# Optimization experiments

Measured on AMD Instinct MI355X. Metric: run time of the kernel, lower is better.

Reference implementation:

```python
import jax, jax.numpy as jnp
import numpy as np

B, LQ, LK = 64, 128, 1024
E, H = 768, 6
HD = E // H            # 128
D2 = HD // 2           # 64
LNUM = 2
QD, KD = 768, 768
EPS = 1e-5


def _gn(x, g, b):
    # torch.nn.GroupNorm(H, E) on 2D input [N, E]: normalize per group of HD channels
    N = x.shape[0]
    xg = x.reshape(N, H, HD)
    m = xg.mean(-1, keepdims=True)
    v = xg.var(-1, keepdims=True)
    xn = ((xg - m) / jnp.sqrt(v + EPS)).reshape(N, E)
    return xn * g + b


def _ln(x, g, b):
    m = x.mean(-1, keepdims=True)
    v = x.var(-1, keepdims=True)
    return (x - m) / jnp.sqrt(v + EPS) * g + b


def setup_inputs() -> dict:
    key = jax.random.key(0)
    ks = iter(jax.random.split(key, 64))
    def rn(shape, s=0.02):
        return jax.random.normal(next(ks), shape, dtype=jnp.float32) * s
    L = LNUM
    inp = {}
    inp['q_feat'] = jax.random.normal(next(ks), (B, LQ, QD), dtype=jnp.float32)
    inp['k_feats'] = jax.random.normal(next(ks), (B, LK, KD), dtype=jnp.float32)
    inp['q_mask'] = jnp.ones((B, LQ), jnp.float32)
    inp['k_mask'] = jnp.ones((B, LK), jnp.float32)
    # per-layer projections (stacked along layer axis)
    inp['Wq'] = rn((L, QD, E)); inp['bq'] = jnp.zeros((L, E)); inp['gq_g'] = jnp.ones((L, E)); inp['gq_b'] = jnp.zeros((L, E))
    inp['Wk'] = rn((L, KD, E)); inp['bk'] = jnp.zeros((L, E)); inp['gk_g'] = jnp.ones((L, E)); inp['gk_b'] = jnp.zeros((L, E))
    inp['Wv1'] = rn((L, QD, E)); inp['bv1'] = jnp.zeros((L, E)); inp['g1_g'] = jnp.ones((L, E)); inp['g1_b'] = jnp.zeros((L, E))
    inp['Wv2'] = rn((L, KD, E)); inp['bv2'] = jnp.zeros((L, E)); inp['g2_g'] = jnp.ones((L, E)); inp['g2_b'] = jnp.zeros((L, E))
    # inner Attention net (per layer)
    inp['Wab'] = rn((L, HD, D2)); inp['bab'] = jnp.zeros((L, D2))
    inp['Wal'] = rn((L, D2, 1)); inp['bal'] = jnp.zeros((L, 1))
    inp['Wac'] = rn((L, D2, HD)); inp['bac'] = jnp.zeros((L, HD))
    # bifeat_emb + layer norms (layer_num-1 of them)
    inp['Wbi'] = rn((L - 1, 2 * E, E)); inp['bbi'] = jnp.zeros((L - 1, E))
    inp['lnb_g'] = jnp.ones((L - 1, E)); inp['lnb_b'] = jnp.zeros((L - 1, E))
    # final proj + layernorm
    inp['Wp'] = rn((E * L + QD, E)); inp['bp'] = jnp.zeros((E,))
    inp['ln_g'] = jnp.ones((E,)); inp['ln_b'] = jnp.zeros((E,))
    return inp


def _bilinear_attention(q, k, kmask, p):
    (Wq, bq, gqg, gqb, Wk, bk, gkg, gkb, Wv1, bv1, g1g, g1b,
     Wv2, bv2, g2g, g2b, Wab, bab, Wal, bal, Wac, bac) = p
    Bb = q.shape[0]
    Lk = k.shape[1]
    qp = _gn(jnp.tanh(q @ Wq + bq), gqg, gqb).reshape(Bb, H, HD)      # [B,H,HD]
    v1 = _gn(jnp.tanh(q @ Wv1 + bv1), g1g, g1b).reshape(Bb, H, HD)
    kf = k.reshape(-1, k.shape[-1])
    kp = _gn(jnp.tanh(kf @ Wk + bk), gkg, gkb).reshape(Bb, Lk, H, HD).transpose(0, 2, 1, 3)   # [B,H,Lk,HD]
    v2 = _gn(jnp.tanh(kf @ Wv2 + bv2), g2g, g2b).reshape(Bb, Lk, H, HD).transpose(0, 2, 1, 3)
    att_map = qp[:, :, None, :] * kp                                  # [B,H,Lk,HD] bilinear map
    basic = jax.nn.relu(att_map @ Wab + bab)                          # [B,H,Lk,D2]
    mext = kmask[:, None, :, None]                                    # [B,1,Lk,1]
    pool = (basic * mext).sum(2) / mext.sum(2)                        # masked mean -> [B,H,D2]
    a_s = (basic @ Wal + bal)[..., 0]                                 # [B,H,Lk]
    a_s = jnp.where(kmask[:, None, :] == 0, -1e9, a_s)
    a_s = jax.nn.softmax(a_s, axis=-1)
    a_c = jax.nn.sigmoid(pool @ Wac + bac)                            # [B,H,HD] channel gate
    v2a = jnp.einsum('bhl,bhld->bhd', a_s, v2)
    return (v1 * v2a * a_c).reshape(Bb, E)


def reference(q_feat, k_feats, q_mask, k_mask,
              Wq, bq, gq_g, gq_b, Wk, bk, gk_g, gk_b,
              Wv1, bv1, g1_g, g1_b, Wv2, bv2, g2_g, g2_b,
              Wab, bab, Wal, bal, Wac, bac,
              Wbi, bbi, lnb_g, lnb_b, Wp, bp, ln_g, ln_b):
    qm = q_mask[..., None]
    q = (q_feat * qm).sum(1) / qm.sum(1)                              # masked mean pool -> [B,QD]
    feats = [q]
    k = k_feats
    for i in range(LNUM):
        p = (Wq[i], bq[i], gq_g[i], gq_b[i], Wk[i], bk[i], gk_g[i], gk_b[i],
             Wv1[i], bv1[i], g1_g[i], g1_b[i], Wv2[i], bv2[i], g2_g[i], g2_b[i],
             Wab[i], bab[i], Wal[i], bal[i], Wac[i], bac[i])
        q = _bilinear_attention(q, k, k_mask, p)                      # dropout = identity (eval)
        feats.append(q)
        if i < LNUM - 1:
            cat = jnp.concatenate([jnp.broadcast_to(q[:, None, :], k.shape), k], axis=-1)
            k = _ln(jax.nn.relu(cat @ Wbi[i] + bbi[i]) + k, lnb_g[i], lnb_b[i])
    out = _ln(jnp.concatenate(feats, axis=-1) @ Wp + bp, ln_g, ln_b)
    return out
```

## Files before the change

kernel.cpp:

```cpp
#include <hip/hip_runtime.h>
#include <math.h>

#define DEVI static __device__ __forceinline__

typedef unsigned short u16;
typedef __attribute__((ext_vector_type(8))) short short8;
typedef __attribute__((ext_vector_type(4))) float f32x4;

DEVI float bf2f(u16 u) { union { float f; unsigned int i; } c; c.i = ((unsigned int)u) << 16; return c.f; }
DEVI u16 f2bf(float f) {
  union { float f; unsigned int i; } c; c.f = f;
  unsigned int r = c.i + 0x7FFFu + ((c.i >> 16) & 1u);
  return (u16)(r >> 16);
}

DEVI float ftanh(float x) {
  float e = __expf(2.f * x);
  return 1.f - 2.f * __builtin_amdgcn_rcpf(e + 1.f);
}

DEVI void gld16(const u16* g, u16* l) {
  __builtin_amdgcn_global_load_lds((const __attribute__((address_space(1))) unsigned int*)g,
                                   (__attribute__((address_space(3))) unsigned int*)l, 16, 0, 0);
}

#define BB 64
#define LQN 128
#define LKN 1024
#define EN 768
#define HN 6
#define HDN 128
#define D2N 64
#define EPSV 1e-5f

#define NB_CONV 3072
#define NB_TW5 2880
#define NB_WAB 16
#define NB_UV 96
#define NB_PQ 64
#define NB_MS 64
#define NB_PREP (NB_CONV + NB_TW5 + NB_WAB + NB_UV + NB_PQ + NB_MS)

__global__ __launch_bounds__(256) void prep_kernel(
    const float* __restrict__ k_feats, u16* __restrict__ kf,
    const float* __restrict__ Wk, const float* __restrict__ Wv2,
    const float* __restrict__ Wbi, const float* __restrict__ lnb_g,
    u16* __restrict__ WkvT, u16* __restrict__ WbiT,
    const float* __restrict__ Wab, u16* __restrict__ WabT,
    const float* __restrict__ lnb_b, const float* __restrict__ bkL1,
    const float* __restrict__ bv2L1, float* __restrict__ uvec,
    float* __restrict__ vbvec,
    const float* __restrict__ qf, const float* __restrict__ qm,
    float* __restrict__ q_cur, float* __restrict__ feats,
    const float* __restrict__ km, float* __restrict__ msum) {
  __shared__ float ls[1056];
  int b = blockIdx.x, t = threadIdx.x;

  if (b < NB_CONV) {
    size_t n8 = (size_t)BB * LKN * EN / 8;
    for (size_t i = (size_t)b * 256 + t; i < n8; i += (size_t)NB_CONV * 256) {
      float4 a = ((const float4*)k_feats)[2 * i];
      float4 c = ((const float4*)k_feats)[2 * i + 1];
      short8 o;
      o[0] = (short)f2bf(a.x); o[1] = (short)f2bf(a.y); o[2] = (short)f2bf(a.z); o[3] = (short)f2bf(a.w);
      o[4] = (short)f2bf(c.x); o[5] = (short)f2bf(c.y); o[6] = (short)f2bf(c.z); o[7] = (short)f2bf(c.w);
      *(short8*)&kf[i * 8] = o;
    }
    return;
  }
  b -= NB_CONV;
  if (b < NB_TW5) {
    int z = b / 576, rem = b % 576;
    int kb = (rem / 24) * 32, nb = (rem % 24) * 32;
    const float* src;
    u16* dst;
    bool fold = (z == 1) || (z == 3);
    if (z < 2) { src = Wk + (size_t)z * EN * EN; dst = WkvT + (size_t)z * 1536 * EN; }
    else if (z < 4) { src = Wv2 + (size_t)(z - 2) * EN * EN; dst = WkvT + (size_t)(z - 2) * 1536 * EN + (size_t)EN * EN; }
    else { src = Wbi + (size_t)EN * EN; dst = WbiT; }
    int tx = t & 31, ty = t >> 5;
    for (int j = 0; j < 32; j += 8) {
      float v = src[(size_t)(kb + ty + j) * EN + nb + tx];
      if (fold) v *= lnb_g[kb + ty + j];
      ls[(ty + j) * 33 + tx] = v;
    }
    __syncthreads();
    for (int j = 0; j < 32; j += 8)
      dst[(size_t)(nb + ty + j) * EN + kb + tx] = f2bf(ls[tx * 33 + ty + j]);
    return;
  }
  b -= NB_TW5;
  if (b < NB_WAB) {
    int z = b / 8, rem = b % 8;
    int kb = (rem / 2) * 32, nb = (rem % 2) * 32;
    const float* src = Wab + (size_t)z * HDN * D2N;
    u16* dst = WabT + (size_t)z * D2N * HDN;
    int tx = t & 31, ty = t >> 5;
    for (int j = 0; j < 32; j += 8)
      ls[(ty + j) * 33 + tx] = src[(size_t)(kb + ty + j) * D2N + nb + tx];
    __syncthreads();
    for (int j = 0; j < 32; j += 8)
      dst[(size_t)(nb + ty + j) * HDN + kb + tx] = f2bf(ls[tx * 33 + ty + j]);
    return;
  }
  b -= NB_WAB;
  if (b < NB_UV) {
    float* pu = ls;
    float* pv = ls + 272;
    int col = t & 15, ks = t >> 4;
    int c = b * 16 + col;
    int part = c >= EN;
    int cc = part ? c - EN : c;
    const float* W = (part ? Wv2 : Wk) + (size_t)EN * EN;
    float u = 0.f, vb = 0.f;
    for (int k = ks * 48; k < ks * 48 + 48; ++k) {
      float w = W[(size_t)k * EN + cc];
      u += lnb_g[k] * w;
      vb += lnb_b[k] * w;
    }
    pu[ks * 17 + col] = u; pv[ks * 17 + col] = vb;
    __syncthreads();
    if (t < 16) {
      int c2 = b * 16 + t;
      int part2 = c2 >= EN;
      int cc2 = part2 ? c2 - EN : c2;
      float su = 0.f, sv = 0.f;
#pragma unroll
      for (int s = 0; s < 16; ++s) { su += pu[s * 17 + t]; sv += pv[s * 17 + t]; }
      sv += part2 ? bv2L1[cc2] : bkL1[cc2];
      uvec[c2] = su;
      vbvec[c2] = sv;
    }
    return;
  }
  b -= NB_UV;
  if (b < NB_PQ) {
    float s0 = 0.f, s1 = 0.f, s2 = 0.f, ms = 0.f;
    for (int l = 0; l < LQN; ++l) {
      float w = qm[b * LQN + l];
      const float* row = qf + ((size_t)b * LQN + l) * EN;
      s0 += row[t] * w; s1 += row[t + 256] * w; s2 += row[t + 512] * w;
      ms += w;
    }
    float inv = 1.f / ms;
    q_cur[(size_t)b * EN + t] = s0 * inv;
    q_cur[(size_t)b * EN + t + 256] = s1 * inv;
    q_cur[(size_t)b * EN + t + 512] = s2 * inv;
    feats[(size_t)b * 3 * EN + t] = s0 * inv;
    feats[(size_t)b * 3 * EN + t + 256] = s1 * inv;
    feats[(size_t)b * 3 * EN + t + 512] = s2 * inv;
    return;
  }
  b -= NB_PQ;
  {
    float s = 0.f;
    for (int l = t; l < LKN; l += 256) s += km[b * LKN + l];
    ls[t] = s; __syncthreads();
    for (int o = 128; o > 0; o >>= 1) { if (t < o) ls[t] += ls[t + o]; __syncthreads(); }
    if (t == 0) msum[b] = ls[0];
  }
}

__global__ __launch_bounds__(768) void qside2_kernel(
    const float* __restrict__ q_in,
    const float* __restrict__ W0, const float* __restrict__ b0,
    const float* __restrict__ g0, const float* __restrict__ bb0, float* __restrict__ o0,
    const float* __restrict__ W1, const float* __restrict__ b1,
    const float* __restrict__ g1, const float* __restrict__ bb1, float* __restrict__ o1,
    const float* __restrict__ W2, const float* __restrict__ b2, float* __restrict__ o2) {
  __shared__ float qs[EN];
  __shared__ float ys[EN];
  __shared__ float mh[HN], rh[HN];
  int t = threadIdx.x, b = blockIdx.x, which = blockIdx.y;
  const float* W = which == 0 ? W0 : (which == 1 ? W1 : W2);
  const float* bvec = which == 0 ? b0 : (which == 1 ? b1 : b2);
  qs[t] = q_in[(size_t)b * EN + t];
  __syncthreads();
  float acc = 0.f;
  for (int k = 0; k < EN; ++k) acc += qs[k] * W[(size_t)k * EN + t];
  if (which == 2) {
    o2[(size_t)b * EN + t] = acc + bvec[t];
    return;
  }
  const float* g = which ? g1 : g0;
  const float* bb = which ? bb1 : bb0;
  float* outp = which ? o1 : o0;
  float y = tanhf(acc + bvec[t]);
  ys[t] = y; __syncthreads();
  if (t < HN) {
    float s = 0.f, s2 = 0.f;
    for (int d = 0; d < HDN; ++d) { float v = ys[t * HDN + d]; s += v; s2 += v * v; }
    float m = s * (1.f / HDN), var = s2 * (1.f / HDN) - m * m;
    mh[t] = m; rh[t] = rsqrtf(var + EPSV);
  }
  __syncthreads();
  int h = t >> 7;
  outp[(size_t)b * EN + t] = (y - mh[h]) * rh[h] * g[t] + bb[t];
}

template <bool LNF>
__global__ __launch_bounds__(256, 4) void gemm_proj(
    const u16* __restrict__ A, const u16* __restrict__ BT,
    const float* __restrict__ bias_k, const float* __restrict__ g_k,
    const float* __restrict__ bb_k, const float* __restrict__ qp,
    const float* __restrict__ bias_v, const float* __restrict__ g_v,
    const float* __restrict__ bb_v, u16* __restrict__ out_v,
    const u16* __restrict__ Wab_g, const float* __restrict__ bab_g,
    const float* __restrict__ Wal_g, const float* __restrict__ bal_g,
    const float* __restrict__ kmask, float* __restrict__ s_out,
    float* __restrict__ pool_part,
    const float2* __restrict__ rowpart, const float* __restrict__ uvec,
    const float* __restrict__ vbvec) {
  const int K = EN;
  __shared__ __align__(16) u16 SM[16384];
  __shared__ float part2[128][2][2];
  __shared__ float pool_sh[4][64];
  __shared__ float2 rs_sh[128];
  u16* As = SM;
  u16* Bs = SM + 8192;
  int t = threadIdx.x;
  int w = t >> 6, lane = t & 63;
  int wm = w >> 1, wn = w & 1;

  int bid = blockIdx.x;
  int swz = ((bid & 7) * 768) + (bid >> 3);
  int rowT = swz / 12, cT = swz % 12;
  int rowBase = rowT << 7;

  if constexpr (LNF) {
    if (t < 128) {
      float s = 0.f, s2 = 0.f;
#pragma unroll
      for (int i = 0; i < 6; ++i) {
        float2 p = rowpart[(size_t)i * (BB * LKN) + rowBase + t];
        s += p.x; s2 += p.y;
      }
      float mm = s * (1.f / EN);
      float var = s2 * (1.f / EN) - mm * mm;
      float rstd = rsqrtf(var + EPSV);
      rs_sh[t] = make_float2(rstd, -mm * rstd);
    }
  }

  int koff = (((lane & 3) ^ ((lane >> 3) & 3)) << 3);
  const u16* gA = A + (size_t)(rowBase + (w << 5) + (lane >> 2)) * K + koff;
  const u16* gB = BT + (size_t)((cT << 7) + (w << 5) + (lane >> 2)) * K + koff;

  int lrow = lane & 15, kq = lane >> 4;
  int sOff = ((kq ^ ((lrow >> 1) & 3)) << 3);
  f32x4 acc[4][4] = {};

  u16* lA0b = As + (w << 10);
  u16* lB0b = Bs + (w << 10);
  u16* lA1b = As + 4096 + (w << 10);
  u16* lB1b = Bs + 4096 + (w << 10);

#define PROJ_PREF(LA, LB, k0) \
    { gld16(gA + (k0), LA); gld16(gA + (size_t)16 * K + (k0), LA + 512); \
      gld16(gB + (k0), LB); gld16(gB + (size_t)16 * K + (k0), LB + 512); }

#define PROJ_STEP(BASE) \
    { short8 af[4], bf[4]; \
      _Pragma("unroll") \
      for (int m = 0; m < 4; ++m) \
        af[m] = *(const short8*)&As[(BASE) + ((wm * 64 + m * 16 + lrow) << 5) + sOff]; \
      _Pragma("unroll") \
      for (int n = 0; n < 4; ++n) \
        bf[n] = *(const short8*)&Bs[(BASE) + ((wn * 64 + n * 16 + lrow) << 5) + sOff]; \
      _Pragma("unroll") \
      for (int m = 0; m < 4; ++m) \
        _Pragma("unroll") \
        for (int n = 0; n < 4; ++n) \
          acc[m][n] = __builtin_amdgcn_mfma_f32_16x16x32_bf16(af[m], bf[n], acc[m][n], 0, 0, 0); }

  PROJ_PREF(lA0b, lB0b, 0)
#pragma unroll 1
  for (int p = 0; p < 12; ++p) {
    __syncthreads();
    PROJ_PREF(lA1b, lB1b, (2 * p + 1) << 5)
    PROJ_STEP(0)
    __syncthreads();
    if (p < 11) PROJ_PREF(lA0b, lB0b, (2 * p + 2) << 5)
    PROJ_STEP(4096)
  }
#undef PROJ_PREF
#undef PROJ_STEP

  __syncthreads();

  const int which = cT >= 6;
  const int ecol = ((which ? cT - 6 : cT) << 7);
  const float* bias = which ? bias_v : bias_k;
  const int bidx = rowBase >> 10;

  if constexpr (LNF) {
    float un[4], vbn[4];
#pragma unroll
    for (int n = 0; n < 4; ++n) {
      int cc = (cT << 7) + wn * 64 + n * 16 + lrow;
      un[n] = uvec[cc]; vbn[n] = vbvec[cc];
    }
#pragma unroll
    for (int m = 0; m < 4; ++m)
#pragma unroll
      for (int j = 0; j < 4; ++j) {
        int row = wm * 64 + m * 16 + kq * 4 + j;
        float2 st = rs_sh[row];
#pragma unroll
        for (int n = 0; n < 4; ++n) {
          float y = ftanh(st.x * acc[m][n][j] + st.y * un[n] + vbn[n]);
          int c = wn * 64 + n * 16 + lrow;
          int sl = c >> 3;
          int so = ((sl & 7) ^ (row & 7)) | (sl & 8);
          SM[row * 128 + (so << 3) + (c & 7)] = f2bf(y);
        }
      }
  } else {
    float biasv[4];
#pragma unroll
    for (int n = 0; n < 4; ++n)
      biasv[n] = bias[ecol + wn * 64 + n * 16 + lrow];
#pragma unroll
    for (int m = 0; m < 4; ++m)
#pragma unroll
      for (int j = 0; j < 4; ++j) {
        int row = wm * 64 + m * 16 + kq * 4 + j;
#pragma unroll
        for (int n = 0; n < 4; ++n) {
          float y = ftanh(acc[m][n][j] + biasv[n]);
          int c = wn * 64 + n * 16 + lrow;
          int sl = c >> 3;
          int so = ((sl & 7) ^ (row & 7)) | (sl & 8);
          SM[row * 128 + (so << 3) + (c & 7)] = f2bf(y);
        }
      }
  }
  __syncthreads();

  {
    int row = t >> 1, ch = t & 1;
    short8 yv8[8];
    float s = 0.f, s2 = 0.f;
#pragma unroll
    for (int s8 = 0; s8 < 8; ++s8) {
      int sl = (ch << 3) + s8;
      int so = ((sl & 7) ^ (row & 7)) | (sl & 8);
      yv8[s8] = *(const short8*)&SM[row * 128 + (so << 3)];
#pragma unroll
      for (int i = 0; i < 8; ++i) {
        float y = bf2f((u16)yv8[s8][i]);
        s += y; s2 += y * y;
      }
    }
    part2[row][ch][0] = s; part2[row][ch][1] = s2;
    __syncthreads();
    float ssum = part2[row][0][0] + part2[row][1][0];
    float q2 = part2[row][0][1] + part2[row][1][1];
    float mean = ssum * (1.f / 128.f);
    float var = q2 * (1.f / 128.f) - mean * mean;
    float rstd = rsqrtf(var + EPSV);
    const float* gp = which ? g_v : g_k;
    const float* bbp = which ? bb_v : bb_k;
    size_t R = (size_t)rowBase + row;
#pragma unroll
    for (int s8 = 0; s8 < 8; ++s8) {
      int sl = (ch << 3) + s8;
      int so = ((sl & 7) ^ (row & 7)) | (sl & 8);
      int e0 = ecol + (sl << 3);
      float4 g0 = *(const float4*)&gp[e0];
      float4 g1 = *(const float4*)&gp[e0 + 4];
      float4 b0 = *(const float4*)&bbp[e0];
      float4 b1 = *(const float4*)&bbp[e0 + 4];
      float gg[8] = {g0.x, g0.y, g0.z, g0.w, g1.x, g1.y, g1.z, g1.w};
      float bv8[8] = {b0.x, b0.y, b0.z, b0.w, b1.x, b1.y, b1.z, b1.w};
      float ov[8];
#pragma unroll
      for (int i = 0; i < 8; ++i)
        ov[i] = (bf2f((u16)yv8[s8][i]) - mean) * rstd * gg[i] + bv8[i];
      if (!which) {
        float4 q0 = *(const float4*)&qp[(size_t)bidx * EN + e0];
        float4 q1 = *(const float4*)&qp[(size_t)bidx * EN + e0 + 4];
        float qq[8] = {q0.x, q0.y, q0.z, q0.w, q1.x, q1.y, q1.z, q1.w};
#pragma unroll
        for (int i = 0; i < 8; ++i) ov[i] *= qq[i];
      }
      short8 o8;
#pragma unroll
      for (int i = 0; i < 8; ++i) o8[i] = (short)f2bf(ov[i]);
      if (which) *(short8*)&out_v[R * EN + e0] = o8;
      else       *(short8*)&SM[row * 128 + (so << 3)] = o8;
    }
  }
  if (which) return;
  __syncthreads();

  const int h = cT;
  const int lt = (rowBase >> 7) & 7;
  f32x4 acc2[2][4] = {};
#pragma unroll
  for (int ks = 0; ks < 4; ++ks) {
    short8 af2[2], bf2[4];
#pragma unroll
    for (int mm = 0; mm < 2; ++mm) {
      int l = w * 32 + mm * 16 + lrow;
      int sl = ks * 4 + kq;
      int so = ((sl & 7) ^ (l & 7)) | (sl & 8);
      af2[mm] = *(const short8*)&SM[l * 128 + so * 8];
    }
#pragma unroll
    for (int n = 0; n < 4; ++n)
      bf2[n] = *(const short8*)&Wab_g[(size_t)(n * 16 + lrow) * 128 + ks * 32 + kq * 8];
#pragma unroll
    for (int mm = 0; mm < 2; ++mm)
#pragma unroll
      for (int n = 0; n < 4; ++n)
        acc2[mm][n] = __builtin_amdgcn_mfma_f32_16x16x32_bf16(af2[mm], bf2[n], acc2[mm][n], 0, 0, 0);
  }

  float wv[4], bv[4];
#pragma unroll
  for (int n = 0; n < 4; ++n) { int c = n * 16 + lrow; wv[n] = Wal_g[c]; bv[n] = bab_g[c]; }
  float kmv[2][4];
  const float* km = kmask + (size_t)bidx * LKN + lt * 128;
#pragma unroll
  for (int mm = 0; mm < 2; ++mm)
#pragma unroll
    for (int j = 0; j < 4; ++j) kmv[mm][j] = km[w * 32 + mm * 16 + kq * 4 + j];
  float balv = bal_g[0];
  float pp[4] = {0.f, 0.f, 0.f, 0.f};
#pragma unroll
  for (int mm = 0; mm < 2; ++mm)
#pragma unroll
    for (int j = 0; j < 4; ++j) {
      float sp = 0.f;
#pragma unroll
      for (int n = 0; n < 4; ++n) {
        float bsv = fmaxf(acc2[mm][n][j] + bv[n], 0.f);
        sp += bsv * wv[n];
        pp[n] += bsv * kmv[mm][j];
      }
      sp += __shfl_xor(sp, 1, 64);
      sp += __shfl_xor(sp, 2, 64);
      sp += __shfl_xor(sp, 4, 64);
      sp += __shfl_xor(sp, 8, 64);
      if (lrow == 0)
        s_out[(((size_t)bidx * HN + h) << 10) + lt * 128 + w * 32 + mm * 16 + kq * 4 + j] = sp + balv;
    }
#pragma unroll
  for (int n = 0; n < 4; ++n) {
    pp[n] += __shfl_xor(pp[n], 16, 64);
    pp[n] += __shfl_xor(pp[n], 32, 64);
  }
  if (lane < 16) {
#pragma unroll
    for (int n = 0; n < 4; ++n) pool_sh[w][n * 16 + lane] = pp[n];
  }
  __syncthreads();
  if (t < 64) {
    float p = pool_sh[0][t] + pool_sh[1][t] + pool_sh[2][t] + pool_sh[3][t];
    pool_part[((((size_t)bidx * HN + h) << 3) + lt) * 64 + t] = p;
  }
}

__global__ __launch_bounds__(256, 4) void gemm_bilin(
    const u16* __restrict__ A, const u16* __restrict__ BT,
    const float* __restrict__ biasB, const u16* __restrict__ resid,
    u16* __restrict__ out, float2* __restrict__ rowpart) {
  const int K = EN;
  __shared__ __align__(16) u16 SM[16384];
  __shared__ float bps[128], bpq[128];
  u16* As = SM;
  u16* Bs = SM + 8192;
  int t = threadIdx.x;
  int w = t >> 6, lane = t & 63;
  int wm = w >> 1, wn = w & 1;

  int bid = blockIdx.x;
  int swz = ((bid & 7) * 384) + (bid >> 3);
  int rowT = swz / 6, cT = swz % 6;
  int rowBase = rowT << 7;
  int colBase = cT << 7;

  int koff = (((lane & 3) ^ ((lane >> 3) & 3)) << 3);
  const u16* gA = A + (size_t)(rowBase + (w << 5) + (lane >> 2)) * K + koff;
  const u16* gB = BT + (size_t)(colBase + (w << 5) + (lane >> 2)) * K + koff;

  int lrow = lane & 15, kq = lane >> 4;
  int sOff = ((kq ^ ((lrow >> 1) & 3)) << 3);
  f32x4 acc[4][4] = {};

  u16* lA0b = As + (w << 10);
  u16* lB0b = Bs + (w << 10);
  u16* lA1b = As + 4096 + (w << 10);
  u16* lB1b = Bs + 4096 + (w << 10);

#define BIL_PREF(LA, LB, k0) \
    { gld16(gA + (k0), LA); gld16(gA + (size_t)16 * K + (k0), LA + 512); \
      gld16(gB + (k0), LB); gld16(gB + (size_t)16 * K + (k0), LB + 512); }

#define BIL_STEP(BASE) \
    { short8 af[4], bf[4]; \
      _Pragma("unroll") \
      for (int m = 0; m < 4; ++m) \
        af[m] = *(const short8*)&As[(BASE) + ((wm * 64 + m * 16 + lrow) << 5) + sOff]; \
      _Pragma("unroll") \
      for (int n = 0; n < 4; ++n) \
        bf[n] = *(const short8*)&Bs[(BASE) + ((wn * 64 + n * 16 + lrow) << 5) + sOff]; \
      _Pragma("unroll") \
      for (int m = 0; m < 4; ++m) \
        _Pragma("unroll") \
        for (int n = 0; n < 4; ++n) \
          acc[m][n] = __builtin_amdgcn_mfma_f32_16x16x32_bf16(af[m], bf[n], acc[m][n], 0, 0, 0); }

  BIL_PREF(lA0b, lB0b, 0)
#pragma unroll 1
  for (int p = 0; p < 12; ++p) {
    __syncthreads();
    BIL_PREF(lA1b, lB1b, (2 * p + 1) << 5)
    BIL_STEP(0)
    __syncthreads();
    if (p < 11) BIL_PREF(lA0b, lB0b, (2 * p + 2) << 5)
    BIL_STEP(4096)
  }
#undef BIL_PREF
#undef BIL_STEP

  __syncthreads();

  const int bidx = rowBase >> 10;
  {
    float qv[4];
#pragma unroll
    for (int n = 0; n < 4; ++n)
      qv[n] = biasB[(size_t)bidx * EN + colBase + wn * 64 + n * 16 + lrow];
#pragma unroll
    for (int m = 0; m < 4; ++m)
#pragma unroll
      for (int j = 0; j < 4; ++j) {
        int row = wm * 64 + m * 16 + kq * 4 + j;
#pragma unroll
        for (int n = 0; n < 4; ++n) {
          float y = fmaxf(acc[m][n][j] + qv[n], 0.f);
          int c = wn * 64 + n * 16 + lrow;
          int sl = c >> 3;
          int so = ((sl & 7) ^ (row & 7)) | (sl & 8);
          SM[row * 128 + (so << 3) + (c & 7)] = f2bf(y);
        }
      }
  }
  __syncthreads();

  {
    int row = t >> 1, ch = t & 1;
    size_t R = (size_t)rowBase + row;
    float s = 0.f, s2 = 0.f;
#pragma unroll
    for (int s8 = 0; s8 < 8; ++s8) {
      int sl = (ch << 3) + s8;
      int so = ((sl & 7) ^ (row & 7)) | (sl & 8);
      short8 yv = *(const short8*)&SM[row * 128 + (so << 3)];
      int e0 = colBase + (sl << 3);
      short8 rv = *(const short8*)&resid[R * EN + e0];
      short8 o8;
#pragma unroll
      for (int i = 0; i < 8; ++i) {
        u16 zb = f2bf(bf2f((u16)yv[i]) + bf2f((u16)rv[i]));
        o8[i] = (short)zb;
        float zf = bf2f(zb);
        s += zf; s2 += zf * zf;
      }
      *(short8*)&out[R * EN + e0] = o8;
    }
    if (ch == 1) { bps[row] = s; bpq[row] = s2; }
    __syncthreads();
    if (ch == 0)
      rowpart[(size_t)cT * (BB * LKN) + R] = make_float2(s + bps[row], s2 + bpq[row]);
  }
}

__global__ __launch_bounds__(256) void attn_fin(
    const float* __restrict__ s_in, const float* __restrict__ kmask,
    const float* __restrict__ msum, const float* __restrict__ pool_part,
    const float* __restrict__ Wac, const float* __restrict__ bac,
    const u16* __restrict__ v2, const float* __restrict__ v1,
    float* __restrict__ q_cur, float* __restrict__ feats, int slot) {
  __shared__ float as_sh[LKN];
  __shared__ float red[256];
  __shared__ float red8[16][129];
  __shared__ float pool_sh[64];
  __shared__ float ac_sh[128];
  int t = threadIdx.x;
  int h = blockIdx.x, b = blockIdx.y;
  const float* sb = s_in + (((size_t)b * HN + h) << 10);
  const float* km = kmask + (size_t)b * LKN;
  float v[4];
  float mx = -1e30f;
#pragma unroll
  for (int j = 0; j < 4; ++j) {
    int l = t * 4 + j;
    float x = sb[l];
    if (km[l] == 0.f) x = -1e9f;
    v[j] = x; mx = fmaxf(mx, x);
  }
  red[t] = mx; __syncthreads();
  for (int o = 128; o > 0; o >>= 1) { if (t < o) red[t] = fmaxf(red[t], red[t + o]); __syncthreads(); }
  float mxv = red[0];
  __syncthreads();
  float sum = 0.f;
#pragma unroll
  for (int j = 0; j < 4; ++j) { v[j] = __expf(v[j] - mxv); sum += v[j]; }
  red[t] = sum; __syncthreads();
  for (int o = 128; o > 0; o >>= 1) { if (t < o) red[t] += red[t + o]; __syncthreads(); }
  float inv = 1.f / red[0];
#pragma unroll
  for (int j = 0; j < 4; ++j) as_sh[t * 4 + j] = v[j] * inv;
  if (t < 64) {
    float p = 0.f;
    for (int lt = 0; lt < 8; ++lt)
      p += pool_part[((((size_t)b * HN + h) << 3) + lt) * 64 + t];
    pool_sh[t] = p / msum[b];
  }
  __syncthreads();
  if (t < 128) {
    float a = 0.f;
    for (int j = 0; j < 64; ++j) a += pool_sh[j] * Wac[j * HDN + t];
    ac_sh[t] = 1.f / (1.f + __expf(-(a + bac[t])));
  }
  __syncthreads();
  {
    int o = t & 15, sl = t >> 4;
    const u16* vb = v2 + ((size_t)b * LKN) * EN + h * HDN + o * 8;
    float a8[8] = {};
    for (int l = sl; l < LKN; l += 16) {
      short8 u = *(const short8*)&vb[(size_t)l * EN];
      float wgt = as_sh[l];
#pragma unroll
      for (int i = 0; i < 8; ++i) a8[i] += wgt * bf2f((u16)u[i]);
    }
#pragma unroll
    for (int i = 0; i < 8; ++i) red8[sl][o * 8 + i] = a8[i];
  }
  __syncthreads();
  if (t < 128) {
    float va = 0.f;
#pragma unroll
    for (int s = 0; s < 16; ++s) va += red8[s][t];
    size_t idx = (size_t)b * EN + h * HDN + t;
    float q = v1[idx] * va * ac_sh[t];
    q_cur[idx] = q;
    feats[(size_t)b * 3 * EN + slot * EN + h * HDN + t] = q;
  }
}

__global__ __launch_bounds__(768) void final_kernel(
    const float* __restrict__ feats, const float* __restrict__ Wp,
    const float* __restrict__ bp, const float* __restrict__ g,
    const float* __restrict__ bb, float* __restrict__ outp) {
  __shared__ float fs[2304];
  __shared__ float red[24];
  __shared__ float mv[2];
  int t = threadIdx.x, b = blockIdx.x;
  fs[t] = feats[(size_t)b * 2304 + t];
  fs[t + 768] = feats[(size_t)b * 2304 + 768 + t];
  fs[t + 1536] = feats[(size_t)b * 2304 + 1536 + t];
  __syncthreads();
  float acc = 0.f;
  for (int k = 0; k < 2304; ++k) acc += fs[k] * Wp[(size_t)k * EN + t];
  float y = acc + bp[t];
  float s = y, s2 = y * y;
  for (int o = 32; o > 0; o >>= 1) { s += __shfl_down(s, o, 64); s2 += __shfl_down(s2, o, 64); }
  int wid = t >> 6, lane = t & 63;
  if (lane == 0) { red[wid] = s; red[12 + wid] = s2; }
  __syncthreads();
  if (t == 0) {
    float ts = 0.f, ts2 = 0.f;
    for (int i = 0; i < 12; ++i) { ts += red[i]; ts2 += red[12 + i]; }
    float m = ts * (1.f / EN), var = ts2 * (1.f / EN) - m * m;
    mv[0] = m; mv[1] = rsqrtf(var + EPSV);
  }
  __syncthreads();
  outp[(size_t)b * EN + t] = (y - mv[0]) * mv[1] * g[t] + bb[t];
}

extern "C" void kernel_launch(void* const* d_in, const int* in_sizes, int n_in,
                              void* d_out, int out_size, void* d_ws, size_t ws_size,
                              hipStream_t stream) {
  const float* q_feat = (const float*)d_in[0];
  const float* k_feats = (const float*)d_in[1];
  const float* q_mask = (const float*)d_in[2];
  const float* k_mask = (const float*)d_in[3];
  const float* Wq = (const float*)d_in[4];
  const float* bq = (const float*)d_in[5];
  const float* gq_g = (const float*)d_in[6];
  const float* gq_b = (const float*)d_in[7];
  const float* Wk = (const float*)d_in[8];
  const float* bk = (const float*)d_in[9];
  const float* gk_g = (const float*)d_in[10];
  const float* gk_b = (const float*)d_in[11];
  const float* Wv1 = (const float*)d_in[12];
  const float* bv1 = (const float*)d_in[13];
  const float* g1_g = (const float*)d_in[14];
  const float* g1_b = (const float*)d_in[15];
  const float* Wv2 = (const float*)d_in[16];
  const float* bv2 = (const float*)d_in[17];
  const float* g2_g = (const float*)d_in[18];
  const float* g2_b = (const float*)d_in[19];
  const float* Wab = (const float*)d_in[20];
  const float* bab = (const float*)d_in[21];
  const float* Wal = (const float*)d_in[22];
  const float* bal = (const float*)d_in[23];
  const float* Wac = (const float*)d_in[24];
  const float* bac = (const float*)d_in[25];
  const float* Wbi = (const float*)d_in[26];
  const float* bbi = (const float*)d_in[27];
  const float* lnb_g = (const float*)d_in[28];
  const float* lnb_b = (const float*)d_in[29];
  const float* Wp = (const float*)d_in[30];
  const float* bp = (const float*)d_in[31];
  const float* ln_g = (const float*)d_in[32];
  const float* ln_b = (const float*)d_in[33];
  float* out = (float*)d_out;
  (void)in_sizes; (void)n_in; (void)out_size; (void)ws_size;

  char* ws = (char*)d_ws;
  size_t off = 0;
  auto alloc = [&](size_t bytes) -> char* {
    char* p = ws + off;
    off += (bytes + 255) & ~(size_t)255;
    return p;
  };
  const size_t MK = (size_t)BB * LKN;
  u16* kf = (u16*)alloc(MK * EN * 2);
  u16* zbuf = (u16*)alloc(MK * EN * 2);
  u16* v2b = (u16*)alloc(MK * EN * 2);
  u16* WkvT = (u16*)alloc((size_t)2 * 1536 * EN * 2);
  u16* WbiT = (u16*)alloc((size_t)EN * EN * 2);
  u16* WabT = (u16*)alloc((size_t)2 * D2N * HDN * 2);
  float* feats = (float*)alloc((size_t)BB * 3 * EN * 4);
  float* q_cur = (float*)alloc((size_t)BB * EN * 4);
  float* qp = (float*)alloc((size_t)BB * EN * 4);
  float* v1 = (float*)alloc((size_t)BB * EN * 4);
  float* qpart = (float*)alloc((size_t)BB * EN * 4);
  float* sbuf = (float*)alloc((size_t)BB * HN * LKN * 4);
  float* poolp = (float*)alloc((size_t)BB * HN * 8 * D2N * 4);
  float* msum = (float*)alloc((size_t)BB * 4);
  float2* rowpart = (float2*)alloc((size_t)6 * MK * 8);
  float* uvec = (float*)alloc(1536 * 4);
  float* vbvec = (float*)alloc(1536 * 4);

  prep_kernel<<<NB_PREP, 256, 0, stream>>>(
      k_feats, kf, Wk, Wv2, Wbi, lnb_g, WkvT, WbiT, Wab, WabT,
      lnb_b, bk + EN, bv2 + EN, uvec, vbvec,
      q_feat, q_mask, q_cur, feats, k_mask, msum);

  qside2_kernel<<<dim3(BB, 2), 768, 0, stream>>>(
      q_cur, Wq, bq, gq_g, gq_b, qp,
      Wv1, bv1, g1_g, g1_b, v1, nullptr, nullptr, nullptr);
  gemm_proj<false><<<6144, 256, 0, stream>>>(
      kf, WkvT, bk, gk_g, gk_b, qp,
      bv2, g2_g, g2_b, v2b,
      WabT, bab, Wal, bal, k_mask, sbuf, poolp,
      nullptr, nullptr, nullptr);
  attn_fin<<<dim3(HN, BB), 256, 0, stream>>>(
      sbuf, k_mask, msum, poolp, Wac, bac, v2b, v1, q_cur, feats, 1);

  qside2_kernel<<<dim3(BB, 3), 768, 0, stream>>>(
      q_cur, Wq + (size_t)EN * EN, bq + EN, gq_g + EN, gq_b + EN, qp,
      Wv1 + (size_t)EN * EN, bv1 + EN, g1_g + EN, g1_b + EN, v1,
      Wbi, bbi, qpart);
  gemm_bilin<<<3072, 256, 0, stream>>>(kf, WbiT, qpart, kf, zbuf, rowpart);
  gemm_proj<true><<<6144, 256, 0, stream>>>(
      zbuf, WkvT + (size_t)1536 * EN, bk + EN, gk_g + EN, gk_b + EN, qp,
      bv2 + EN, g2_g + EN, g2_b + EN, v2b,
      WabT + (size_t)D2N * HDN, bab + D2N, Wal + D2N, bal + 1, k_mask, sbuf, poolp,
      rowpart, uvec, vbvec);
  attn_fin<<<dim3(HN, BB), 256, 0, stream>>>(
      sbuf, k_mask, msum, poolp, Wac + (size_t)D2N * HDN, bac + HDN, v2b, v1, q_cur, feats, 2);

  final_kernel<<<BB, EN, 0, stream>>>(feats, Wp, bp, ln_g, ln_b, out);
}
```

Before: 934.3 us.

## Use 8 waves per block in projection and bilinear GEMMs

Doubles the threads per block in gemm_proj and gemm_bilin from 256 to 512, so each wave computes a 64x32 sub-tile instead of 64x64 of the 128x128 output tile. Each wave now issues one global-to-LDS load per operand per stage, and the LayerNorm, epilogue and attention-score reductions are rewritten for 4 column chunks and 8 waves. The aim is more waves in flight to hide memory latency and fewer accumulator registers per wave. The cost is lower MFMA-to-LDS-read reuse per wave and more block-wide synchronisation.

```diff
diff --git a/kernel.cpp b/kernel.cpp
--- a/kernel.cpp
+++ b/kernel.cpp
@@ -199,7 +199,7 @@
 }
 
 template <bool LNF>
-__global__ __launch_bounds__(256, 4) void gemm_proj(
+__global__ __launch_bounds__(512, 8) void gemm_proj(
     const u16* __restrict__ A, const u16* __restrict__ BT,
     const float* __restrict__ bias_k, const float* __restrict__ g_k,
     const float* __restrict__ bb_k, const float* __restrict__ qp,
@@ -213,14 +213,14 @@
     const float* __restrict__ vbvec) {
   const int K = EN;
   __shared__ __align__(16) u16 SM[16384];
-  __shared__ float part2[128][2][2];
-  __shared__ float pool_sh[4][64];
+  __shared__ float part2[128][4][2];
+  __shared__ float pool_sh[8][64];
   __shared__ float2 rs_sh[128];
   u16* As = SM;
   u16* Bs = SM + 8192;
   int t = threadIdx.x;
   int w = t >> 6, lane = t & 63;
-  int wm = w >> 1, wn = w & 1;
+  int wm = w >> 2, wn = w & 3;
 
   int bid = blockIdx.x;
   int swz = ((bid & 7) * 768) + (bid >> 3);
@@ -243,34 +243,33 @@
   }
 
   int koff = (((lane & 3) ^ ((lane >> 3) & 3)) << 3);
-  const u16* gA = A + (size_t)(rowBase + (w << 5) + (lane >> 2)) * K + koff;
-  const u16* gB = BT + (size_t)((cT << 7) + (w << 5) + (lane >> 2)) * K + koff;
+  const u16* gA = A + (size_t)(rowBase + (w << 4) + (lane >> 2)) * K + koff;
+  const u16* gB = BT + (size_t)((cT << 7) + (w << 4) + (lane >> 2)) * K + koff;
 
   int lrow = lane & 15, kq = lane >> 4;
   int sOff = ((kq ^ ((lrow >> 1) & 3)) << 3);
-  f32x4 acc[4][4] = {};
-
-  u16* lA0b = As + (w << 10);
-  u16* lB0b = Bs + (w << 10);
-  u16* lA1b = As + 4096 + (w << 10);
-  u16* lB1b = Bs + 4096 + (w << 10);
+  f32x4 acc[4][2] = {};
+
+  u16* lA0b = As + (w << 9);
+  u16* lB0b = Bs + (w << 9);
+  u16* lA1b = As + 4096 + (w << 9);
+  u16* lB1b = Bs + 4096 + (w << 9);
 
 #define PROJ_PREF(LA, LB, k0) \
-    { gld16(gA + (k0), LA); gld16(gA + (size_t)16 * K + (k0), LA + 512); \
-      gld16(gB + (k0), LB); gld16(gB + (size_t)16 * K + (k0), LB + 512); }
+    { gld16(gA + (k0), LA); gld16(gB + (k0), LB); }
 
 #define PROJ_STEP(BASE) \
-    { short8 af[4], bf[4]; \
+    { short8 af[4], bf[2]; \
       _Pragma("unroll") \
       for (int m = 0; m < 4; ++m) \
         af[m] = *(const short8*)&As[(BASE) + ((wm * 64 + m * 16 + lrow) << 5) + sOff]; \
       _Pragma("unroll") \
-      for (int n = 0; n < 4; ++n) \
-        bf[n] = *(const short8*)&Bs[(BASE) + ((wn * 64 + n * 16 + lrow) << 5) + sOff]; \
+      for (int n = 0; n < 2; ++n) \
+        bf[n] = *(const short8*)&Bs[(BASE) + ((wn * 32 + n * 16 + lrow) << 5) + sOff]; \
       _Pragma("unroll") \
       for (int m = 0; m < 4; ++m) \
         _Pragma("unroll") \
-        for (int n = 0; n < 4; ++n) \
+        for (int n = 0; n < 2; ++n) \
           acc[m][n] = __builtin_amdgcn_mfma_f32_16x16x32_bf16(af[m], bf[n], acc[m][n], 0, 0, 0); }
 
   PROJ_PREF(lA0b, lB0b, 0)
@@ -294,10 +293,10 @@
   const int bidx = rowBase >> 10;
 
   if constexpr (LNF) {
-    float un[4], vbn[4];
-#pragma unroll
-    for (int n = 0; n < 4; ++n) {
-      int cc = (cT << 7) + wn * 64 + n * 16 + lrow;
+    float un[2], vbn[2];
+#pragma unroll
+    for (int n = 0; n < 2; ++n) {
+      int cc = (cT << 7) + wn * 32 + n * 16 + lrow;
       un[n] = uvec[cc]; vbn[n] = vbvec[cc];
     }
 #pragma unroll
@@ -307,28 +306,28 @@
         int row = wm * 64 + m * 16 + kq * 4 + j;
         float2 st = rs_sh[row];
 #pragma unroll
-        for (int n = 0; n < 4; ++n) {
+        for (int n = 0; n < 2; ++n) {
           float y = ftanh(st.x * acc[m][n][j] + st.y * un[n] + vbn[n]);
-          int c = wn * 64 + n * 16 + lrow;
+          int c = wn * 32 + n * 16 + lrow;
           int sl = c >> 3;
           int so = ((sl & 7) ^ (row & 7)) | (sl & 8);
           SM[row * 128 + (so << 3) + (c & 7)] = f2bf(y);
         }
       }
   } else {
-    float biasv[4];
-#pragma unroll
-    for (int n = 0; n < 4; ++n)
-      biasv[n] = bias[ecol + wn * 64 + n * 16 + lrow];
+    float biasv[2];
+#pragma unroll
+    for (int n = 0; n < 2; ++n)
+      biasv[n] = bias[ecol + wn * 32 + n * 16 + lrow];
 #pragma unroll
     for (int m = 0; m < 4; ++m)
 #pragma unroll
       for (int j = 0; j < 4; ++j) {
         int row = wm * 64 + m * 16 + kq * 4 + j;
 #pragma unroll
-        for (int n = 0; n < 4; ++n) {
+        for (int n = 0; n < 2; ++n) {
           float y = ftanh(acc[m][n][j] + biasv[n]);
-          int c = wn * 64 + n * 16 + lrow;
+          int c = wn * 32 + n * 16 + lrow;
           int sl = c >> 3;
           int so = ((sl & 7) ^ (row & 7)) | (sl & 8);
           SM[row * 128 + (so << 3) + (c & 7)] = f2bf(y);
@@ -338,12 +337,12 @@
   __syncthreads();
 
   {
-    int row = t >> 1, ch = t & 1;
-    short8 yv8[8];
+    int row = t >> 2, ch = t & 3;
+    short8 yv8[4];
     float s = 0.f, s2 = 0.f;
 #pragma unroll
-    for (int s8 = 0; s8 < 8; ++s8) {
-      int sl = (ch << 3) + s8;
+    for (int s8 = 0; s8 < 4; ++s8) {
+      int sl = (ch << 2) + s8;
       int so = ((sl & 7) ^ (row & 7)) | (sl & 8);
       yv8[s8] = *(const short8*)&SM[row * 128 + (so << 3)];
 #pragma unroll
@@ -354,8 +353,8 @@
     }
     part2[row][ch][0] = s; part2[row][ch][1] = s2;
     __syncthreads();
-    float ssum = part2[row][0][0] + part2[row][1][0];
-    float q2 = part2[row][0][1] + part2[row][1][1];
+    float ssum = part2[row][0][0] + part2[row][1][0] + part2[row][2][0] + part2[row][3][0];
+    float q2 = part2[row][0][1] + part2[row][1][1] + part2[row][2][1] + part2[row][3][1];
     float mean = ssum * (1.f / 128.f);
     float var = q2 * (1.f / 128.f) - mean * mean;
     float rstd = rsqrtf(var + EPSV);
@@ -363,8 +362,8 @@
     const float* bbp = which ? bb_v : bb_k;
     size_t R = (size_t)rowBase + row;
 #pragma unroll
-    for (int s8 = 0; s8 < 8; ++s8) {
-      int sl = (ch << 3) + s8;
+    for (int s8 = 0; s8 < 4; ++s8) {
+      int sl = (ch << 2) + s8;
       int so = ((sl & 7) ^ (row & 7)) | (sl & 8);
       int e0 = ecol + (sl << 3);
       float4 g0 = *(const float4*)&gp[e0];
@@ -396,56 +395,49 @@
 
   const int h = cT;
   const int lt = (rowBase >> 7) & 7;
-  f32x4 acc2[2][4] = {};
+  f32x4 acc2[4] = {};
 #pragma unroll
   for (int ks = 0; ks < 4; ++ks) {
-    short8 af2[2], bf2[4];
-#pragma unroll
-    for (int mm = 0; mm < 2; ++mm) {
-      int l = w * 32 + mm * 16 + lrow;
+    short8 af2, bf2[4];
+    {
+      int l = w * 16 + lrow;
       int sl = ks * 4 + kq;
       int so = ((sl & 7) ^ (l & 7)) | (sl & 8);
-      af2[mm] = *(const short8*)&SM[l * 128 + so * 8];
+      af2 = *(const short8*)&SM[l * 128 + so * 8];
     }
 #pragma unroll
     for (int n = 0; n < 4; ++n)
       bf2[n] = *(const short8*)&Wab_g[(size_t)(n * 16 + lrow) * 128 + ks * 32 + kq * 8];
 #pragma unroll
-    for (int mm = 0; mm < 2; ++mm)
-#pragma unroll
-      for (int n = 0; n < 4; ++n)
-        acc2[mm][n] = __builtin_amdgcn_mfma_f32_16x16x32_bf16(af2[mm], bf2[n], acc2[mm][n], 0, 0, 0);
+    for (int n = 0; n < 4; ++n)
+      acc2[n] = __builtin_amdgcn_mfma_f32_16x16x32_bf16(af2, bf2[n], acc2[n], 0, 0, 0);
   }
 
   float wv[4], bv[4];
 #pragma unroll
   for (int n = 0; n < 4; ++n) { int c = n * 16 + lrow; wv[n] = Wal_g[c]; bv[n] = bab_g[c]; }
-  float kmv[2][4];
+  float kmv[4];
   const float* km = kmask + (size_t)bidx * LKN + lt * 128;
 #pragma unroll
-  for (int mm = 0; mm < 2; ++mm)
-#pragma unroll
-    for (int j = 0; j < 4; ++j) kmv[mm][j] = km[w * 32 + mm * 16 + kq * 4 + j];
+  for (int j = 0; j < 4; ++j) kmv[j] = km[w * 16 + kq * 4 + j];
   float balv = bal_g[0];
   float pp[4] = {0.f, 0.f, 0.f, 0.f};
 #pragma unroll
-  for (int mm = 0; mm < 2; ++mm)
-#pragma unroll
-    for (int j = 0; j < 4; ++j) {
-      float sp = 0.f;
-#pragma unroll
-      for (int n = 0; n < 4; ++n) {
-        float bsv = fmaxf(acc2[mm][n][j] + bv[n], 0.f);
-        sp += bsv * wv[n];
-        pp[n] += bsv * kmv[mm][j];
-      }
-      sp += __shfl_xor(sp, 1, 64);
-      sp += __shfl_xor(sp, 2, 64);
-      sp += __shfl_xor(sp, 4, 64);
-      sp += __shfl_xor(sp, 8, 64);
-      if (lrow == 0)
-        s_out[(((size_t)bidx * HN + h) << 10) + lt * 128 + w * 32 + mm * 16 + kq * 4 + j] = sp + balv;
-    }
+  for (int j = 0; j < 4; ++j) {
+    float sp = 0.f;
+#pragma unroll
+    for (int n = 0; n < 4; ++n) {
+      float bsv = fmaxf(acc2[n][j] + bv[n], 0.f);
+      sp += bsv * wv[n];
+      pp[n] += bsv * kmv[j];
+    }
+    sp += __shfl_xor(sp, 1, 64);
+    sp += __shfl_xor(sp, 2, 64);
+    sp += __shfl_xor(sp, 4, 64);
+    sp += __shfl_xor(sp, 8, 64);
+    if (lrow == 0)
+      s_out[(((size_t)bidx * HN + h) << 10) + lt * 128 + w * 16 + kq * 4 + j] = sp + balv;
+  }
 #pragma unroll
   for (int n = 0; n < 4; ++n) {
     pp[n] += __shfl_xor(pp[n], 16, 64);
@@ -457,23 +449,25 @@
   }
   __syncthreads();
   if (t < 64) {
-    float p = pool_sh[0][t] + pool_sh[1][t] + pool_sh[2][t] + pool_sh[3][t];
+    float p = 0.f;
+#pragma unroll
+    for (int ww = 0; ww < 8; ++ww) p += pool_sh[ww][t];
     pool_part[((((size_t)bidx * HN + h) << 3) + lt) * 64 + t] = p;
   }
 }
 
-__global__ __launch_bounds__(256, 4) void gemm_bilin(
+__global__ __launch_bounds__(512, 8) void gemm_bilin(
     const u16* __restrict__ A, const u16* __restrict__ BT,
     const float* __restrict__ biasB, const u16* __restrict__ resid,
     u16* __restrict__ out, float2* __restrict__ rowpart) {
   const int K = EN;
   __shared__ __align__(16) u16 SM[16384];
-  __shared__ float bps[128], bpq[128];
+  __shared__ float bps[128][4], bpq[128][4];
   u16* As = SM;
   u16* Bs = SM + 8192;
   int t = threadIdx.x;
   int w = t >> 6, lane = t & 63;
-  int wm = w >> 1, wn = w & 1;
+  int wm = w >> 2, wn = w & 3;
 
   int bid = blockIdx.x;
   int swz = ((bid & 7) * 384) + (bid >> 3);
@@ -482,34 +476,33 @@
   int colBase = cT << 7;
 
   int koff = (((lane & 3) ^ ((lane >> 3) & 3)) << 3);
-  const u16* gA = A + (size_t)(rowBase + (w << 5) + (lane >> 2)) * K + koff;
-  const u16* gB = BT + (size_t)(colBase + (w << 5) + (lane >> 2)) * K + koff;
+  const u16* gA = A + (size_t)(rowBase + (w << 4) + (lane >> 2)) * K + koff;
+  const u16* gB = BT + (size_t)(colBase + (w << 4) + (lane >> 2)) * K + koff;
 
   int lrow = lane & 15, kq = lane >> 4;
   int sOff = ((kq ^ ((lrow >> 1) & 3)) << 3);
-  f32x4 acc[4][4] = {};
-
-  u16* lA0b = As + (w << 10);
-  u16* lB0b = Bs + (w << 10);
-  u16* lA1b = As + 4096 + (w << 10);
-  u16* lB1b = Bs + 4096 + (w << 10);
+  f32x4 acc[4][2] = {};
+
+  u16* lA0b = As + (w << 9);
+  u16* lB0b = Bs + (w << 9);
+  u16* lA1b = As + 4096 + (w << 9);
+  u16* lB1b = Bs + 4096 + (w << 9);
 
 #define BIL_PREF(LA, LB, k0) \
-    { gld16(gA + (k0), LA); gld16(gA + (size_t)16 * K + (k0), LA + 512); \
-      gld16(gB + (k0), LB); gld16(gB + (size_t)16 * K + (k0), LB + 512); }
+    { gld16(gA + (k0), LA); gld16(gB + (k0), LB); }
 
 #define BIL_STEP(BASE) \
-    { short8 af[4], bf[4]; \
+    { short8 af[4], bf[2]; \
       _Pragma("unroll") \
       for (int m = 0; m < 4; ++m) \
         af[m] = *(const short8*)&As[(BASE) + ((wm * 64 + m * 16 + lrow) << 5) + sOff]; \
       _Pragma("unroll") \
-      for (int n = 0; n < 4; ++n) \
-        bf[n] = *(const short8*)&Bs[(BASE) + ((wn * 64 + n * 16 + lrow) << 5) + sOff]; \
+      for (int n = 0; n < 2; ++n) \
+        bf[n] = *(const short8*)&Bs[(BASE) + ((wn * 32 + n * 16 + lrow) << 5) + sOff]; \
       _Pragma("unroll") \
       for (int m = 0; m < 4; ++m) \
         _Pragma("unroll") \
-        for (int n = 0; n < 4; ++n) \
+        for (int n = 0; n < 2; ++n) \
           acc[m][n] = __builtin_amdgcn_mfma_f32_16x16x32_bf16(af[m], bf[n], acc[m][n], 0, 0, 0); }
 
   BIL_PREF(lA0b, lB0b, 0)
@@ -529,19 +522,19 @@
 
   const int bidx = rowBase >> 10;
   {
-    float qv[4];
-#pragma unroll
-    for (int n = 0; n < 4; ++n)
-      qv[n] = biasB[(size_t)bidx * EN + colBase + wn * 64 + n * 16 + lrow];
+    float qv[2];
+#pragma unroll
+    for (int n = 0; n < 2; ++n)
+      qv[n] = biasB[(size_t)bidx * EN + colBase + wn * 32 + n * 16 + lrow];
 #pragma unroll
     for (int m = 0; m < 4; ++m)
 #pragma unroll
       for (int j = 0; j < 4; ++j) {
         int row = wm * 64 + m * 16 + kq * 4 + j;
 #pragma unroll
-        for (int n = 0; n < 4; ++n) {
+        for (int n = 0; n < 2; ++n) {
           float y = fmaxf(acc[m][n][j] + qv[n], 0.f);
-          int c = wn * 64 + n * 16 + lrow;
+          int c = wn * 32 + n * 16 + lrow;
           int sl = c >> 3;
           int so = ((sl & 7) ^ (row & 7)) | (sl & 8);
           SM[row * 128 + (so << 3) + (c & 7)] = f2bf(y);
@@ -551,12 +544,12 @@
   __syncthreads();
 
   {
-    int row = t >> 1, ch = t & 1;
+    int row = t >> 2, ch = t & 3;
     size_t R = (size_t)rowBase + row;
     float s = 0.f, s2 = 0.f;
 #pragma unroll
-    for (int s8 = 0; s8 < 8; ++s8) {
-      int sl = (ch << 3) + s8;
+    for (int s8 = 0; s8 < 4; ++s8) {
+      int sl = (ch << 2) + s8;
       int so = ((sl & 7) ^ (row & 7)) | (sl & 8);
       short8 yv = *(const short8*)&SM[row * 128 + (so << 3)];
       int e0 = colBase + (sl << 3);
@@ -571,10 +564,12 @@
       }
       *(short8*)&out[R * EN + e0] = o8;
     }
-    if (ch == 1) { bps[row] = s; bpq[row] = s2; }
+    bps[row][ch] = s; bpq[row][ch] = s2;
     __syncthreads();
     if (ch == 0)
-      rowpart[(size_t)cT * (BB * LKN) + R] = make_float2(s + bps[row], s2 + bpq[row]);
+      rowpart[(size_t)cT * (BB * LKN) + R] = make_float2(
+          bps[row][0] + bps[row][1] + bps[row][2] + bps[row][3],
+          bpq[row][0] + bpq[row][1] + bpq[row][2] + bpq[row][3]);
   }
 }
 
@@ -756,7 +751,7 @@
   qside2_kernel<<<dim3(BB, 2), 768, 0, stream>>>(
       q_cur, Wq, bq, gq_g, gq_b, qp,
       Wv1, bv1, g1_g, g1_b, v1, nullptr, nullptr, nullptr);
-  gemm_proj<false><<<6144, 256, 0, stream>>>(
+  gemm_proj<false><<<6144, 512, 0, stream>>>(
       kf, WkvT, bk, gk_g, gk_b, qp,
       bv2, g2_g, g2_b, v2b,
       WabT, bab, Wal, bal, k_mask, sbuf, poolp,
@@ -768,8 +763,8 @@
       q_cur, Wq + (size_t)EN * EN, bq + EN, gq_g + EN, gq_b + EN, qp,
       Wv1 + (size_t)EN * EN, bv1 + EN, g1_g + EN, g1_b + EN, v1,
       Wbi, bbi, qpart);
-  gemm_bilin<<<3072, 256, 0, stream>>>(kf, WbiT, qpart, kf, zbuf, rowpart);
-  gemm_proj<true><<<6144, 256, 0, stream>>>(
+  gemm_bilin<<<3072, 512, 0, stream>>>(kf, WbiT, qpart, kf, zbuf, rowpart);
+  gemm_proj<true><<<6144, 512, 0, stream>>>(
       zbuf, WkvT + (size_t)1536 * EN, bk + EN, gk_g + EN, gk_b + EN, qp,
       bv2 + EN, g2_g + EN, g2_b + EN, v2b,
       WabT + (size_t)D2N * HDN, bab + D2N, Wal + D2N, bal + 1, k_mask, sbuf, poolp,
```

New measurement: 1.093 ms. 17.0% more time.

## Give each wave private LDS tiles to remove block barriers in GEMM main loops

Applied to the files above, without the earlier changes.

Both projection and bilinear GEMMs now have each wave load its own 64-row A and B slices into a private LDS region. Waves then sync only with their own loads through vmcnt waits instead of block-wide __syncthreads. This doubles LDS use and halves the occupancy target to 2 blocks. It also duplicates global loads, since waves sharing a row or column tile each fetch it. The aim is to remove barrier stalls and let waves run independently, at the cost of more memory traffic and lower occupancy.

```diff
diff --git a/kernel.cpp b/kernel.cpp
--- a/kernel.cpp
+++ b/kernel.cpp
@@ -199,7 +199,7 @@
 }
 
 template <bool LNF>
-__global__ __launch_bounds__(256, 4) void gemm_proj(
+__global__ __launch_bounds__(256, 2) void gemm_proj(
     const u16* __restrict__ A, const u16* __restrict__ BT,
     const float* __restrict__ bias_k, const float* __restrict__ g_k,
     const float* __restrict__ bb_k, const float* __restrict__ qp,
@@ -212,12 +212,10 @@
     const float2* __restrict__ rowpart, const float* __restrict__ uvec,
     const float* __restrict__ vbvec) {
   const int K = EN;
-  __shared__ __align__(16) u16 SM[16384];
+  __shared__ __align__(16) u16 SM[32768];
   __shared__ float part2[128][2][2];
   __shared__ float pool_sh[4][64];
   __shared__ float2 rs_sh[128];
-  u16* As = SM;
-  u16* Bs = SM + 8192;
   int t = threadIdx.x;
   int w = t >> 6, lane = t & 63;
   int wm = w >> 1, wn = w & 1;
@@ -243,47 +241,50 @@
   }
 
   int koff = (((lane & 3) ^ ((lane >> 3) & 3)) << 3);
-  const u16* gA = A + (size_t)(rowBase + (w << 5) + (lane >> 2)) * K + koff;
-  const u16* gB = BT + (size_t)((cT << 7) + (w << 5) + (lane >> 2)) * K + koff;
+  const u16* gA = A + (size_t)(rowBase + wm * 64 + (lane >> 2)) * K + koff;
+  const u16* gB = BT + (size_t)((cT << 7) + wn * 64 + (lane >> 2)) * K + koff;
 
   int lrow = lane & 15, kq = lane >> 4;
   int sOff = ((kq ^ ((lrow >> 1) & 3)) << 3);
   f32x4 acc[4][4] = {};
 
-  u16* lA0b = As + (w << 10);
-  u16* lB0b = Bs + (w << 10);
-  u16* lA1b = As + 4096 + (w << 10);
-  u16* lB1b = Bs + 4096 + (w << 10);
-
-#define PROJ_PREF(LA, LB, k0) \
-    { gld16(gA + (k0), LA); gld16(gA + (size_t)16 * K + (k0), LA + 512); \
-      gld16(gB + (k0), LB); gld16(gB + (size_t)16 * K + (k0), LB + 512); }
-
-#define PROJ_STEP(BASE) \
+  u16* myr = SM + (w << 13);
+
+#define PROJ_STAGE(BUFOFS, k0) \
+    { _Pragma("unroll") \
+      for (int g = 0; g < 4; ++g) { \
+        gld16(gA + (size_t)(g * 16) * K + (k0), myr + (BUFOFS) + g * 512); \
+        gld16(gB + (size_t)(g * 16) * K + (k0), myr + (BUFOFS) + 2048 + g * 512); } }
+
+#define PROJ_STEP(BUFOFS) \
     { short8 af[4], bf[4]; \
       _Pragma("unroll") \
       for (int m = 0; m < 4; ++m) \
-        af[m] = *(const short8*)&As[(BASE) + ((wm * 64 + m * 16 + lrow) << 5) + sOff]; \
+        af[m] = *(const short8*)&myr[(BUFOFS) + ((m * 16 + lrow) << 5) + sOff]; \
       _Pragma("unroll") \
       for (int n = 0; n < 4; ++n) \
-        bf[n] = *(const short8*)&Bs[(BASE) + ((wn * 64 + n * 16 + lrow) << 5) + sOff]; \
+        bf[n] = *(const short8*)&myr[(BUFOFS) + 2048 + ((n * 16 + lrow) << 5) + sOff]; \
       _Pragma("unroll") \
       for (int m = 0; m < 4; ++m) \
         _Pragma("unroll") \
         for (int n = 0; n < 4; ++n) \
           acc[m][n] = __builtin_amdgcn_mfma_f32_16x16x32_bf16(af[m], bf[n], acc[m][n], 0, 0, 0); }
 
-  PROJ_PREF(lA0b, lB0b, 0)
+  PROJ_STAGE(0, 0)
 #pragma unroll 1
   for (int p = 0; p < 12; ++p) {
-    __syncthreads();
-    PROJ_PREF(lA1b, lB1b, (2 * p + 1) << 5)
+    PROJ_STAGE(4096, (2 * p + 1) << 5)
+    asm volatile("s_waitcnt vmcnt(8)" ::: "memory");
     PROJ_STEP(0)
-    __syncthreads();
-    if (p < 11) PROJ_PREF(lA0b, lB0b, (2 * p + 2) << 5)
+    if (p < 11) {
+      PROJ_STAGE(0, (2 * p + 2) << 5)
+      asm volatile("s_waitcnt vmcnt(8)" ::: "memory");
+    } else {
+      asm volatile("s_waitcnt vmcnt(0)" ::: "memory");
+    }
     PROJ_STEP(4096)
   }
-#undef PROJ_PREF
+#undef PROJ_STAGE
 #undef PROJ_STEP
 
   __syncthreads();
@@ -462,15 +463,13 @@
   }
 }
 
-__global__ __launch_bounds__(256, 4) void gemm_bilin(
+__global__ __launch_bounds__(256, 2) void gemm_bilin(
     const u16* __restrict__ A, const u16* __restrict__ BT,
     const float* __restrict__ biasB, const u16* __restrict__ resid,
     u16* __restrict__ out, float2* __restrict__ rowpart) {
   const int K = EN;
-  __shared__ __align__(16) u16 SM[16384];
+  __shared__ __align__(16) u16 SM[32768];
   __shared__ float bps[128], bpq[128];
-  u16* As = SM;
-  u16* Bs = SM + 8192;
   int t = threadIdx.x;
   int w = t >> 6, lane = t & 63;
   int wm = w >> 1, wn = w & 1;
@@ -482,47 +481,50 @@
   int colBase = cT << 7;
 
   int koff = (((lane & 3) ^ ((lane >> 3) & 3)) << 3);
-  const u16* gA = A + (size_t)(rowBase + (w << 5) + (lane >> 2)) * K + koff;
-  const u16* gB = BT + (size_t)(colBase + (w << 5) + (lane >> 2)) * K + koff;
+  const u16* gA = A + (size_t)(rowBase + wm * 64 + (lane >> 2)) * K + koff;
+  const u16* gB = BT + (size_t)(colBase + wn * 64 + (lane >> 2)) * K + koff;
 
   int lrow = lane & 15, kq = lane >> 4;
   int sOff = ((kq ^ ((lrow >> 1) & 3)) << 3);
   f32x4 acc[4][4] = {};
 
-  u16* lA0b = As + (w << 10);
-  u16* lB0b = Bs + (w << 10);
-  u16* lA1b = As + 4096 + (w << 10);
-  u16* lB1b = Bs + 4096 + (w << 10);
-
-#define BIL_PREF(LA, LB, k0) \
-    { gld16(gA + (k0), LA); gld16(gA + (size_t)16 * K + (k0), LA + 512); \
-      gld16(gB + (k0), LB); gld16(gB + (size_t)16 * K + (k0), LB + 512); }
-
-#define BIL_STEP(BASE) \
+  u16* myr = SM + (w << 13);
+
+#define BIL_STAGE(BUFOFS, k0) \
+    { _Pragma("unroll") \
+      for (int g = 0; g < 4; ++g) { \
+        gld16(gA + (size_t)(g * 16) * K + (k0), myr + (BUFOFS) + g * 512); \
+        gld16(gB + (size_t)(g * 16) * K + (k0), myr + (BUFOFS) + 2048 + g * 512); } }
+
+#define BIL_STEP(BUFOFS) \
     { short8 af[4], bf[4]; \
       _Pragma("unroll") \
       for (int m = 0; m < 4; ++m) \
-        af[m] = *(const short8*)&As[(BASE) + ((wm * 64 + m * 16 + lrow) << 5) + sOff]; \
+        af[m] = *(const short8*)&myr[(BUFOFS) + ((m * 16 + lrow) << 5) + sOff]; \
       _Pragma("unroll") \
       for (int n = 0; n < 4; ++n) \
-        bf[n] = *(const short8*)&Bs[(BASE) + ((wn * 64 + n * 16 + lrow) << 5) + sOff]; \
+        bf[n] = *(const short8*)&myr[(BUFOFS) + 2048 + ((n * 16 + lrow) << 5) + sOff]; \
       _Pragma("unroll") \
       for (int m = 0; m < 4; ++m) \
         _Pragma("unroll") \
         for (int n = 0; n < 4; ++n) \
           acc[m][n] = __builtin_amdgcn_mfma_f32_16x16x32_bf16(af[m], bf[n], acc[m][n], 0, 0, 0); }
 
-  BIL_PREF(lA0b, lB0b, 0)
+  BIL_STAGE(0, 0)
 #pragma unroll 1
   for (int p = 0; p < 12; ++p) {
-    __syncthreads();
-    BIL_PREF(lA1b, lB1b, (2 * p + 1) << 5)
+    BIL_STAGE(4096, (2 * p + 1) << 5)
+    asm volatile("s_waitcnt vmcnt(8)" ::: "memory");
     BIL_STEP(0)
-    __syncthreads();
-    if (p < 11) BIL_PREF(lA0b, lB0b, (2 * p + 2) << 5)
+    if (p < 11) {
+      BIL_STAGE(0, (2 * p + 2) << 5)
+      asm volatile("s_waitcnt vmcnt(8)" ::: "memory");
+    } else {
+      asm volatile("s_waitcnt vmcnt(0)" ::: "memory");
+    }
     BIL_STEP(4096)
   }
-#undef BIL_PREF
+#undef BIL_STAGE
 #undef BIL_STEP
 
   __syncthreads();
```

Result: slower. 1.181 ms (+26.4%).
